# Performance work log

Measured on AMD Instinct MI355X. Metric: run time of the kernel, lower is better.

## Reference

```python
import jax, jax.numpy as jnp
import numpy as np

B, N, T_OBS, N_HEAD = 64, 512, 8, 4
IN_FEAT = T_OBS * 2          # 16
OUT_FEAT = IN_FEAT * 4       # 64 (GAT out / MLP in)
HID1, HID2 = 1024, 512
S, NSAMP = 2, 20
OUT_DIM = S * NSAMP          # 40


def setup_inputs() -> dict:
    key = jax.random.key(0)
    ks = jax.random.split(key, 12)
    x = jax.random.normal(ks[0], (B, N, T_OBS, 2), dtype=jnp.float32)
    # binary adjacency-style mask over the dense node-node attention
    mask = (jax.random.uniform(ks[1], (B, 1, N, N)) > 0.1).astype(jnp.float32)
    xav = lambda k, shp, fi, fo: jax.random.uniform(k, shp, jnp.float32, -1.0, 1.0) * (1.414 * np.sqrt(6.0 / (fi + fo)))
    w = xav(ks[2], (N_HEAD, IN_FEAT, OUT_FEAT), IN_FEAT, OUT_FEAT)
    a_src = xav(ks[3], (N_HEAD, OUT_FEAT, 1), OUT_FEAT, 1)
    a_dst = xav(ks[4], (N_HEAD, OUT_FEAT, 1), OUT_FEAT, 1)
    bias = jnp.zeros((OUT_FEAT,), jnp.float32)
    lin = lambda k, fi, fo: jax.random.uniform(k, (fi, fo), jnp.float32, -1.0, 1.0) * np.sqrt(1.0 / fi)
    W1 = lin(ks[5], OUT_FEAT, HID1); b1 = jnp.zeros((HID1,), jnp.float32)
    W2 = lin(ks[6], HID1, HID2);     b2 = jnp.zeros((HID2,), jnp.float32)
    W3 = lin(ks[7], HID2, OUT_DIM);  b3 = jnp.zeros((OUT_DIM,), jnp.float32)
    return {"x": x, "mask": mask, "w": w, "a_src": a_src, "a_dst": a_dst,
            "bias": bias, "W1": W1, "b1": b1, "W2": W2, "b2": b2, "W3": W3, "b3": b3}


def reference(x, mask, w, a_src, a_dst, bias, W1, b1, W2, b2, W3, b3):
    b, n = x.shape[0], x.shape[1]
    node = x.reshape(b, n, -1)                                   # [B,N,16]
    # per-head projection: [B,N,16] x [H,16,64] -> [B,H,N,64]
    h_prime = jnp.einsum('bni,hio->bhno', node, w)
    attn_src = jnp.einsum('bhno,ho->bhn', h_prime, a_src[..., 0])
    attn_dst = jnp.einsum('bhno,ho->bhn', h_prime, a_dst[..., 0])
    attn = attn_src[..., :, None] * attn_dst[..., None, :]       # [B,H,N,N] outer product
    attn = jnp.where(attn >= 0, attn, 0.2 * attn)                # leaky_relu(0.2)
    attn = jax.nn.softmax(attn, axis=-1)
    # dropout is identity in eval mode
    attn = attn * mask
    out = jnp.einsum('bhnm,bhmo->bno', attn, h_prime) + bias     # sum over heads fused
    out = out + h_prime.sum(axis=1)                              # skip connection
    # MLP: activation BEFORE each linear (as in original MLP.forward)
    y = out
    for W, bb in ((W1, b1), (W2, b2), (W3, b3)):
        y = jax.nn.relu(y) @ W + bb
    y = y.reshape(b, n, NSAMP, -1)[..., 0:S]                     # [B,N,20,2]
    return jnp.clip(jax.nn.sigmoid(y), 0.01, 0.99)
```

## Files before the change

### kernel.cpp

```cpp
#include <hip/hip_runtime.h>
#include <math.h>

typedef short bf16x8 __attribute__((ext_vector_type(8)));
typedef float f32x4 __attribute__((ext_vector_type(4)));

#define BB 64
#define NN 512
#define NH 4
#define FI 16
#define FO 64
#define HD1 1024
#define HD2 512
#define ODIM 40

__device__ __forceinline__ unsigned short f2bf(float f) {
    unsigned u = __float_as_uint(f);
    u += 0x7fffu + ((u >> 16) & 1u);
    return (unsigned short)(u >> 16);
}
__device__ __forceinline__ unsigned pack2(float a, float b) {
    return (unsigned)f2bf(a) | ((unsigned)f2bf(b) << 16);
}
__device__ __forceinline__ void gload16(const void* g, void* l) {
    __builtin_amdgcn_global_load_lds(
        (const __attribute__((address_space(1))) unsigned int*)g,
        (__attribute__((address_space(3))) unsigned int*)l,
        16, 0, 0);
}

__global__ void k_wa(const float* __restrict__ w, const float* __restrict__ a_src,
                     const float* __restrict__ a_dst, float* __restrict__ wa)
{
    int t = threadIdx.x;
    int h = t >> 4;
    float s = 0.f, d = 0.f;
    for (int o = 0; o < FO; ++o) {
        float wv = w[t*FO + o];
        s = fmaf(wv, a_src[h*FO + o], s);
        d = fmaf(wv, a_dst[h*FO + o], d);
    }
    wa[t] = s; wa[64 + t] = d;
}

__global__ __launch_bounds__(256) void k_proj2(
    const float* __restrict__ x, const float* __restrict__ w,
    const float* __restrict__ bias, const float* __restrict__ wa,
    short* __restrict__ hpT,
    float* __restrict__ asrc, float* __restrict__ adst,
    float* __restrict__ gat)
{
    __shared__ float xS[64][20];
    __shared__ float gS[NH][64][64];
    int b = blockIdx.y;
    int n0 = blockIdx.x * 64;
    int t = threadIdx.x;
    int h = t >> 6, o = t & 63;
    {
        int n = t >> 2, q = t & 3;
        float4 v = *(const float4*)&x[((size_t)b*NN + n0 + n)*FI + q*4];
        *(float4*)&xS[n][q*4] = v;
    }
    float wreg[16];
#pragma unroll
    for (int i = 0; i < FI; ++i) wreg[i] = w[(h*FI + i)*FO + o];
    __syncthreads();

    size_t hbase = ((size_t)(b*NH + h)*FO + o) * NN + n0;
    for (int nc = 0; nc < 8; ++nc) {
        float acc[8];
#pragma unroll
        for (int k = 0; k < 8; ++k) {
            int n = nc*8 + k;
            float4 a0 = *(const float4*)&xS[n][0];
            float4 a1 = *(const float4*)&xS[n][4];
            float4 a2 = *(const float4*)&xS[n][8];
            float4 a3 = *(const float4*)&xS[n][12];
            float sA = fmaf(a0.x, wreg[0], fmaf(a0.y, wreg[1], fmaf(a0.z, wreg[2], a0.w*wreg[3])));
            float sB = fmaf(a1.x, wreg[4], fmaf(a1.y, wreg[5], fmaf(a1.z, wreg[6], a1.w*wreg[7])));
            float sC = fmaf(a2.x, wreg[8], fmaf(a2.y, wreg[9], fmaf(a2.z, wreg[10], a2.w*wreg[11])));
            float sD = fmaf(a3.x, wreg[12], fmaf(a3.y, wreg[13], fmaf(a3.z, wreg[14], a3.w*wreg[15])));
            float s = (sA + sB) + (sC + sD);
            acc[k] = s;
            gS[h][n][o] = s;
        }
        uint4 p;
        p.x = pack2(acc[0], acc[1]); p.y = pack2(acc[2], acc[3]);
        p.z = pack2(acc[4], acc[5]); p.w = pack2(acc[6], acc[7]);
        *(uint4*)&hpT[hbase + nc*8] = p;
    }
    {
        int n = o;
        float vs = 0.f, vd = 0.f;
#pragma unroll
        for (int i = 0; i < FI; ++i) {
            float xv = xS[n][i];
            vs = fmaf(xv, wa[h*FI + i], vs);
            vd = fmaf(xv, wa[64 + h*FI + i], vd);
        }
        asrc[(size_t)(b*NH + h)*NN + n0 + n] = vs;
        adst[(size_t)(b*NH + h)*NN + n0 + n] = vd;
    }
    __syncthreads();
#pragma unroll
    for (int r = 0; r < 16; ++r) {
        int idx = t + r*256;
        int n = idx >> 6, oo = idx & 63;
        float g = bias[oo] + ((gS[0][n][oo] + gS[1][n][oo]) + (gS[2][n][oo] + gS[3][n][oo]));
        gat[((size_t)b*NN + n0 + n)*FO + oo] = g;
    }
}

__global__ __launch_bounds__(256) void k_attn2(
    const short* __restrict__ hpT, const float* __restrict__ mask,
    const float* __restrict__ asrc, const float* __restrict__ adst,
    float* __restrict__ gat)
{
    __shared__ float dS[NH*NN];
    __shared__ char vts[16384];
    __shared__ float dmaxS[NH], dminS[NH];
    int b = blockIdx.y;
    int i0blk = blockIdx.x * 64;
    int t = threadIdx.x;
#pragma unroll
    for (int r = 0; r < 8; ++r) {
        int idx = t + r*256;
        dS[idx] = adst[(size_t)b*(NH*NN) + idx];
    }
    __syncthreads();
    int wv = t >> 6, lane = t & 63;
    {
        float mx = -INFINITY, mn = INFINITY;
        const float* dh = &dS[wv*NN];
#pragma unroll
        for (int q = 0; q < 8; ++q) {
            float v = dh[lane*8 + q];
            mx = fmaxf(mx, v); mn = fminf(mn, v);
        }
#pragma unroll
        for (int off = 1; off < 64; off <<= 1) {
            mx = fmaxf(mx, __shfl_xor(mx, off));
            mn = fminf(mn, __shfl_xor(mn, off));
        }
        if (lane == 0) { dmaxS[wv] = mx; dminS[wv] = mn; }
    }
    __syncthreads();
    int li = lane & 15, kq = lane >> 4;
    int i = i0blk + wv*16 + li;
    float s[NH], m[NH], Ssum[NH];
#pragma unroll
    for (int h = 0; h < NH; ++h) {
        s[h] = asrc[(size_t)(b*NH + h)*NN + i];
        float dm = s[h] >= 0.f ? dmaxS[h] : dminS[h];
        float l = s[h] * dm;
        m[h] = fmaxf(l, 0.2f*l);
        Ssum[h] = 0.f;
    }
    f32x4 accH[NH][4];
#pragma unroll
    for (int h = 0; h < NH; ++h)
#pragma unroll
        for (int ot = 0; ot < 4; ++ot) accH[h][ot] = (f32x4)0.f;

    const float* mrow = &mask[((size_t)b*NN + i)*NN];
    for (int jt = 0; jt < 16; ++jt) {
        int j0 = jt*32;
#pragma unroll
        for (int q = 0; q < 4; ++q) {
            int flatB = wv*4096 + q*1024 + lane*16;
            int row = flatB >> 6;
            int slotS = ((flatB >> 4) & 3) ^ ((row >> 1) & 3);
            const short* src = hpT + ((size_t)b*256 + row)*NN + j0 + slotS*8;
            gload16(src, vts + wv*4096 + q*1024);
        }
        __syncthreads();
        float4 mk0 = *(const float4*)&mrow[j0 + kq*8];
        float4 mk1 = *(const float4*)&mrow[j0 + kq*8 + 4];
        float mk[8] = {mk0.x, mk0.y, mk0.z, mk0.w, mk1.x, mk1.y, mk1.z, mk1.w};
#pragma unroll
        for (int h = 0; h < NH; ++h) {
            float4 d0 = *(const float4*)&dS[h*NN + j0 + kq*8];
            float4 d1 = *(const float4*)&dS[h*NN + j0 + kq*8 + 4];
            float dv[8] = {d0.x,d0.y,d0.z,d0.w,d1.x,d1.y,d1.z,d1.w};
            float u[8];
#pragma unroll
            for (int q = 0; q < 8; ++q) {
                float v = s[h]*dv[q];
                v = fmaxf(v, 0.2f*v);
                u[q] = __expf(v - m[h]);
            }
            Ssum[h] += ((u[0]+u[1]) + (u[2]+u[3])) + ((u[4]+u[5]) + (u[6]+u[7]));
            union { bf16x8 v; unsigned uu[4]; } pf;
#pragma unroll
            for (int q = 0; q < 4; ++q)
                pf.uu[q] = pack2(u[2*q]*mk[2*q], u[2*q+1]*mk[2*q+1]);
#pragma unroll
            for (int ot = 0; ot < 4; ++ot) {
                int row = h*64 + ot*16 + li;
                int slot = kq ^ ((row >> 1) & 3);
                bf16x8 vf = *(bf16x8*)(vts + row*64 + slot*16);
                accH[h][ot] = __builtin_amdgcn_mfma_f32_16x16x32_bf16(pf.v, vf, accH[h][ot], 0, 0, 0);
            }
        }
        __syncthreads();
    }
#pragma unroll
    for (int h = 0; h < NH; ++h) {
        Ssum[h] += __shfl_xor(Ssum[h], 16);
        Ssum[h] += __shfl_xor(Ssum[h], 32);
    }
    float rinv[NH][4];
#pragma unroll
    for (int h = 0; h < NH; ++h)
#pragma unroll
        for (int g = 0; g < 4; ++g)
            rinv[h][g] = 1.0f / __shfl(Ssum[h], kq*4 + g);
#pragma unroll
    for (int ot = 0; ot < 4; ++ot) {
#pragma unroll
        for (int g = 0; g < 4; ++g) {
            int ii = i0blk + wv*16 + kq*4 + g;
            int oo = ot*16 + li;
            size_t ix = ((size_t)b*NN + ii)*FO + oo;
            float add = accH[0][ot][g]*rinv[0][g] + accH[1][ot][g]*rinv[1][g]
                      + accH[2][ot][g]*rinv[2][g] + accH[3][ot][g]*rinv[3][g];
            gat[ix] += add;
        }
    }
}

__global__ __launch_bounds__(256) void k_conv(
    const float* __restrict__ W1, const float* __restrict__ W2, const float* __restrict__ W3,
    short* __restrict__ w1t, short* __restrict__ w2t, short* __restrict__ w3t)
{
    int idx = blockIdx.x * 256 + threadIdx.x;
    if (idx < HD1*FO) {
        int n = idx >> 6, k = idx & 63;
        w1t[idx] = (short)f2bf(W1[k*HD1 + n]);
    } else if (idx < HD1*FO + HD2*HD1) {
        int i2 = idx - HD1*FO;
        int n = i2 >> 10, k = i2 & 1023;
        w2t[i2] = (short)f2bf(W2[k*HD2 + n]);
    } else if (idx < HD1*FO + HD2*HD1 + 48*HD2) {
        int i3 = idx - (HD1*FO + HD2*HD1);
        int n = i3 >> 9, k = i3 & 511;
        w3t[i3] = (short)(n < ODIM ? f2bf(W3[k*ODIM + n]) : 0);
    }
}

__global__ __launch_bounds__(256, 2) void k_mlpA(
    const float* __restrict__ gat,
    const short* __restrict__ w1t, const float* __restrict__ b1,
    short* __restrict__ h1g)
{
    __shared__ char a0b[8192];
    int t = threadIdx.x;
    int lane = t & 63, wave = t >> 6;
    int li = lane & 15, kq = lane >> 4;
    int m0 = blockIdx.x * 64;

    {
        int row = t >> 2, c0 = (t & 3) * 16;
        const float4* g = (const float4*)&gat[(size_t)(m0 + row) * FO + c0];
        float4 v0 = g[0], v1 = g[1], v2 = g[2], v3 = g[3];
        uint4 p0, p1;
        p0.x = pack2(fmaxf(v0.x,0.f), fmaxf(v0.y,0.f));
        p0.y = pack2(fmaxf(v0.z,0.f), fmaxf(v0.w,0.f));
        p0.z = pack2(fmaxf(v1.x,0.f), fmaxf(v1.y,0.f));
        p0.w = pack2(fmaxf(v1.z,0.f), fmaxf(v1.w,0.f));
        p1.x = pack2(fmaxf(v2.x,0.f), fmaxf(v2.y,0.f));
        p1.y = pack2(fmaxf(v2.z,0.f), fmaxf(v2.w,0.f));
        p1.z = pack2(fmaxf(v3.x,0.f), fmaxf(v3.y,0.f));
        p1.w = pack2(fmaxf(v3.z,0.f), fmaxf(v3.w,0.f));
        int base = row*128 + c0*2;
        *(uint4*)(a0b + (base ^ ((row&7)<<4)))      = p0;
        *(uint4*)(a0b + ((base+16) ^ ((row&7)<<4))) = p1;
    }
    __syncthreads();

    for (int c = 0; c < 4; ++c) {
        int n0 = wave * 256 + c * 64;
        f32x4 acc[4][4];
#pragma unroll
        for (int mt = 0; mt < 4; ++mt)
#pragma unroll
            for (int nt = 0; nt < 4; ++nt) acc[mt][nt] = (f32x4)0.f;
#pragma unroll
        for (int ks = 0; ks < 2; ++ks) {
            int k0 = ks * 32;
            bf16x8 xf[4];
#pragma unroll
            for (int mt = 0; mt < 4; ++mt) {
                int row = mt * 16 + li;
                int addr = (row * 128 + k0 * 2 + kq * 16) ^ ((row & 7) << 4);
                xf[mt] = *(bf16x8*)(a0b + addr);
            }
#pragma unroll
            for (int nt = 0; nt < 4; ++nt) {
                int col = n0 + nt * 16 + li;
                bf16x8 wf = *(const bf16x8*)(w1t + col * 64 + k0 + kq * 8);
#pragma unroll
                for (int mt = 0; mt < 4; ++mt)
                    acc[mt][nt] = __builtin_amdgcn_mfma_f32_16x16x32_bf16(wf, xf[mt], acc[mt][nt], 0, 0, 0);
            }
        }
#pragma unroll
        for (int mt = 0; mt < 4; ++mt)
#pragma unroll
            for (int nt = 0; nt < 4; ++nt) {
                int m = mt * 16 + li;
                int nb = n0 + nt * 16 + kq * 4;
                float4 bb = *(const float4*)&b1[nb];
                float v0 = fmaxf(acc[mt][nt][0] + bb.x, 0.f);
                float v1 = fmaxf(acc[mt][nt][1] + bb.y, 0.f);
                float v2 = fmaxf(acc[mt][nt][2] + bb.z, 0.f);
                float v3 = fmaxf(acc[mt][nt][3] + bb.w, 0.f);
                uint2 pw; pw.x = pack2(v0, v1); pw.y = pack2(v2, v3);
                *(uint2*)&h1g[(size_t)(m0 + m) * HD1 + nb] = pw;
            }
    }
}

#define BUFSZ 40960
__global__ __launch_bounds__(512, 2) void k_mlpB(
    const short* __restrict__ h1g,
    const short* __restrict__ w2t, const float* __restrict__ b2,
    const short* __restrict__ w3t, const float* __restrict__ b3,
    float* __restrict__ out)
{
    extern __shared__ char smem[];
    int t = threadIdx.x;
    int lane = t & 63, wave = t >> 6;
    int li = lane & 15, kq = lane >> 4;
    int m0 = blockIdx.x * 128;

    auto STAGE = [&](int i, int ks) {
        char* base = smem + i * BUFSZ;
        {
            int row = wave * 16 + (lane >> 2);
            int slotS = (lane & 3) ^ ((row >> 1) & 3);
            const short* src = h1g + (size_t)(m0 + row) * HD1 + ks * 32 + slotS * 8;
            gload16(src, base + wave * 1024);
        }
#pragma unroll
        for (int q = 0; q < 4; ++q) {
            int flatB = wave * 4096 + q * 1024 + lane * 16;
            int n = flatB >> 6;
            int slotS = ((flatB >> 4) & 3) ^ ((n >> 1) & 3);
            const short* src = w2t + (size_t)n * HD1 + ks * 32 + slotS * 8;
            gload16(src, base + 8192 + wave * 4096 + q * 1024);
        }
    };

    f32x4 acc2[8][4];
#pragma unroll
    for (int mt = 0; mt < 8; ++mt)
#pragma unroll
        for (int nt = 0; nt < 4; ++nt) acc2[mt][nt] = (f32x4)0.f;

    STAGE(0, 0);
    STAGE(1, 1);
    for (int ks = 0; ks < 32; ++ks) {
        int cur = ks & 1;
        if (ks < 31) { asm volatile("s_waitcnt vmcnt(5)" ::: "memory"); }
        else         { asm volatile("s_waitcnt vmcnt(0)" ::: "memory"); }
        __builtin_amdgcn_sched_barrier(0);
        __builtin_amdgcn_s_barrier();
        __builtin_amdgcn_sched_barrier(0);

        char* base = smem + cur * BUFSZ;
        bf16x8 xf[8], wf[4];
#pragma unroll
        for (int mt = 0; mt < 8; ++mt) {
            int m = mt * 16 + li;
            int slot = kq ^ ((m >> 1) & 3);
            xf[mt] = *(bf16x8*)(base + m * 64 + slot * 16);
        }
#pragma unroll
        for (int nt = 0; nt < 4; ++nt) {
            int n = wave * 64 + nt * 16 + li;
            int slot = kq ^ ((n >> 1) & 3);
            wf[nt] = *(bf16x8*)(base + 8192 + n * 64 + slot * 16);
        }
        asm volatile("s_waitcnt lgkmcnt(0)" ::: "memory");
        __builtin_amdgcn_sched_barrier(0);
        __builtin_amdgcn_s_barrier();
        __builtin_amdgcn_sched_barrier(0);
        if (ks < 30) STAGE(cur, ks + 2);

#pragma unroll
        for (int nt = 0; nt < 4; ++nt)
#pragma unroll
            for (int mt = 0; mt < 8; ++mt)
                acc2[mt][nt] = __builtin_amdgcn_mfma_f32_16x16x32_bf16(wf[nt], xf[mt], acc2[mt][nt], 0, 0, 0);
    }
    __syncthreads();

#pragma unroll
    for (int mt = 0; mt < 8; ++mt)
#pragma unroll
        for (int nt = 0; nt < 4; ++nt) {
            int m = mt * 16 + li;
            int nb = wave * 64 + nt * 16 + kq * 4;
            float4 bb = *(const float4*)&b2[nb];
            float v0 = fmaxf(acc2[mt][nt][0] + bb.x, 0.f);
            float v1 = fmaxf(acc2[mt][nt][1] + bb.y, 0.f);
            float v2 = fmaxf(acc2[mt][nt][2] + bb.z, 0.f);
            float v3 = fmaxf(acc2[mt][nt][3] + bb.w, 0.f);
            uint2 pw; pw.x = pack2(v0, v1); pw.y = pack2(v2, v3);
            int addr = (m * 1024 + nb * 2) ^ ((m & 7) << 4);
            *(uint2*)(smem + addr) = pw;
        }
    __syncthreads();

    f32x4 acc3[3];
#pragma unroll
    for (int nt = 0; nt < 3; ++nt) acc3[nt] = (f32x4)0.f;
#pragma unroll
    for (int ks = 0; ks < 16; ++ks) {
        int k0 = ks * 32;
        int m = wave * 16 + li;
        int addr = (m * 1024 + k0 * 2 + kq * 16) ^ ((m & 7) << 4);
        bf16x8 xf = *(bf16x8*)(smem + addr);
#pragma unroll
        for (int nt = 0; nt < 3; ++nt) {
            int col = nt * 16 + li;
            bf16x8 wf = *(const bf16x8*)(w3t + col * 512 + k0 + kq * 8);
            acc3[nt] = __builtin_amdgcn_mfma_f32_16x16x32_bf16(wf, xf, acc3[nt], 0, 0, 0);
        }
    }
#pragma unroll
    for (int nt = 0; nt < 3; ++nt)
#pragma unroll
        for (int g = 0; g < 4; ++g) {
            int n = nt * 16 + kq * 4 + g;
            if (n < ODIM) {
                int m = wave * 16 + li;
                float s = acc3[nt][g] + b3[n];
                s = 1.f / (1.f + __expf(-s));
                s = fminf(fmaxf(s, 0.01f), 0.99f);
                out[(size_t)(m0 + m) * ODIM + n] = s;
            }
        }
}

extern "C" void kernel_launch(void* const* d_in, const int* in_sizes, int n_in,
                              void* d_out, int out_size, void* d_ws, size_t ws_size,
                              hipStream_t stream)
{
    const float* x     = (const float*)d_in[0];
    const float* mask  = (const float*)d_in[1];
    const float* w     = (const float*)d_in[2];
    const float* a_src = (const float*)d_in[3];
    const float* a_dst = (const float*)d_in[4];
    const float* bias  = (const float*)d_in[5];
    const float* W1    = (const float*)d_in[6];
    const float* b1    = (const float*)d_in[7];
    const float* W2    = (const float*)d_in[8];
    const float* b2    = (const float*)d_in[9];
    const float* W3    = (const float*)d_in[10];
    const float* b3    = (const float*)d_in[11];
    float* out = (float*)d_out;

    char* p = (char*)d_ws;
    short* h1g = (short*)p;
    short* hpT = (short*)p;  p += (size_t)BB*NH*FO*NN*2;
    float* asrc = (float*)p; p += (size_t)BB*NH*NN*4;
    float* adst = (float*)p; p += (size_t)BB*NH*NN*4;
    p = (char*)d_ws + (size_t)BB*NN*HD1*2;
    float* gat  = (float*)p; p += (size_t)BB*NN*FO*4;
    short* w1t  = (short*)p; p += (size_t)HD1*FO*2;
    short* w2t  = (short*)p; p += (size_t)HD2*HD1*2;
    short* w3t  = (short*)p; p += (size_t)48*HD2*2;
    float* wa   = (float*)p; p += 128*4;

    k_wa   <<<1, 64, 0, stream>>>(w, a_src, a_dst, wa);
    k_conv <<<(HD1*FO + HD2*HD1 + 48*HD2)/256, 256, 0, stream>>>(W1, W2, W3, w1t, w2t, w3t);
    k_proj2<<<dim3(NN/64, BB), 256, 0, stream>>>(x, w, bias, wa, hpT, asrc, adst, gat);
    k_attn2<<<dim3(NN/64, BB), 256, 0, stream>>>(hpT, mask, asrc, adst, gat);
    k_mlpA <<<BB*NN/64, 256, 0, stream>>>(gat, w1t, b1, h1g);
    k_mlpB <<<BB*NN/128, 512, 131072, stream>>>(h1g, w2t, b2, w3t, b3, out);
}
```

Measured before the change: 167.7 us.

## Pre-layout hpT and W2 in MFMA fragment order, load directly from global

The projection kernel now writes hpT tiled per 32-column block, so the attention kernel can read MFMA B-fragments straight from global memory. This removes the LDS staging and the two block barriers per tile. W2 is likewise converted into a fragment-ordered layout, and k_mlpB loads weight fragments directly into registers two steps ahead, keeping only the activation tile in LDS. The aim is less LDS traffic and fewer barriers. The cost is more global and L2 reads, since each wave reloads the weights itself, plus extra registers. The existing vmcnt(5) wait now has to cover a different mix of outstanding loads.

```diff
diff --git a/kernel.cpp b/kernel.cpp
--- a/kernel.cpp
+++ b/kernel.cpp
@@ -65,7 +65,7 @@
     for (int i = 0; i < FI; ++i) wreg[i] = w[(h*FI + i)*FO + o];
     __syncthreads();
 
-    size_t hbase = ((size_t)(b*NH + h)*FO + o) * NN + n0;
+    short* hb = hpT + (size_t)b * (NH*FO*NN);
     for (int nc = 0; nc < 8; ++nc) {
         float acc[8];
 #pragma unroll
@@ -86,7 +86,8 @@
         uint4 p;
         p.x = pack2(acc[0], acc[1]); p.y = pack2(acc[2], acc[3]);
         p.z = pack2(acc[4], acc[5]); p.w = pack2(acc[6], acc[7]);
-        *(uint4*)&hpT[hbase + nc*8] = p;
+        int jt = (n0 >> 5) + (nc >> 2);
+        *(uint4*)&hb[(size_t)(jt*256 + h*64 + o)*32 + (nc & 3)*8] = p;
     }
     {
         int n = o;
@@ -116,7 +117,6 @@
     float* __restrict__ gat)
 {
     __shared__ float dS[NH*NN];
-    __shared__ char vts[16384];
     __shared__ float dmaxS[NH], dminS[NH];
     int b = blockIdx.y;
     int i0blk = blockIdx.x * 64;
@@ -162,17 +162,9 @@
         for (int ot = 0; ot < 4; ++ot) accH[h][ot] = (f32x4)0.f;
 
     const float* mrow = &mask[((size_t)b*NN + i)*NN];
+    const short* vb = hpT + (size_t)b * (NH*FO*NN);
     for (int jt = 0; jt < 16; ++jt) {
         int j0 = jt*32;
-#pragma unroll
-        for (int q = 0; q < 4; ++q) {
-            int flatB = wv*4096 + q*1024 + lane*16;
-            int row = flatB >> 6;
-            int slotS = ((flatB >> 4) & 3) ^ ((row >> 1) & 3);
-            const short* src = hpT + ((size_t)b*256 + row)*NN + j0 + slotS*8;
-            gload16(src, vts + wv*4096 + q*1024);
-        }
-        __syncthreads();
         float4 mk0 = *(const float4*)&mrow[j0 + kq*8];
         float4 mk1 = *(const float4*)&mrow[j0 + kq*8 + 4];
         float mk[8] = {mk0.x, mk0.y, mk0.z, mk0.w, mk1.x, mk1.y, mk1.z, mk1.w};
@@ -195,13 +187,10 @@
                 pf.uu[q] = pack2(u[2*q]*mk[2*q], u[2*q+1]*mk[2*q+1]);
 #pragma unroll
             for (int ot = 0; ot < 4; ++ot) {
-                int row = h*64 + ot*16 + li;
-                int slot = kq ^ ((row >> 1) & 3);
-                bf16x8 vf = *(bf16x8*)(vts + row*64 + slot*16);
+                bf16x8 vf = *(const bf16x8*)&vb[(size_t)(jt*256 + h*64 + ot*16 + li)*32 + kq*8];
                 accH[h][ot] = __builtin_amdgcn_mfma_f32_16x16x32_bf16(pf.v, vf, accH[h][ot], 0, 0, 0);
             }
         }
-        __syncthreads();
     }
 #pragma unroll
     for (int h = 0; h < NH; ++h) {
@@ -230,7 +219,7 @@
 
 __global__ __launch_bounds__(256) void k_conv(
     const float* __restrict__ W1, const float* __restrict__ W2, const float* __restrict__ W3,
-    short* __restrict__ w1t, short* __restrict__ w2t, short* __restrict__ w3t)
+    short* __restrict__ w1t, short* __restrict__ w2f, short* __restrict__ w3t)
 {
     int idx = blockIdx.x * 256 + threadIdx.x;
     if (idx < HD1*FO) {
@@ -238,8 +227,9 @@
         w1t[idx] = (short)f2bf(W1[k*HD1 + n]);
     } else if (idx < HD1*FO + HD2*HD1) {
         int i2 = idx - HD1*FO;
-        int n = i2 >> 10, k = i2 & 1023;
-        w2t[i2] = (short)f2bf(W2[k*HD2 + n]);
+        int e = i2 & 7, kqq = (i2 >> 3) & 3, n = (i2 >> 5) & 511, ks = i2 >> 14;
+        int k = ks*32 + kqq*8 + e;
+        w2f[i2] = (short)f2bf(W2[k*HD2 + n]);
     } else if (idx < HD1*FO + HD2*HD1 + 48*HD2) {
         int i3 = idx - (HD1*FO + HD2*HD1);
         int n = i3 >> 9, k = i3 & 511;
@@ -320,10 +310,9 @@
     }
 }
 
-#define BUFSZ 40960
 __global__ __launch_bounds__(512, 2) void k_mlpB(
     const short* __restrict__ h1g,
-    const short* __restrict__ w2t, const float* __restrict__ b2,
+    const short* __restrict__ w2f, const float* __restrict__ b2,
     const short* __restrict__ w3t, const float* __restrict__ b3,
     float* __restrict__ out)
 {
@@ -334,22 +323,13 @@
     int m0 = blockIdx.x * 128;
 
     auto STAGE = [&](int i, int ks) {
-        char* base = smem + i * BUFSZ;
-        {
-            int row = wave * 16 + (lane >> 2);
-            int slotS = (lane & 3) ^ ((row >> 1) & 3);
-            const short* src = h1g + (size_t)(m0 + row) * HD1 + ks * 32 + slotS * 8;
-            gload16(src, base + wave * 1024);
-        }
-#pragma unroll
-        for (int q = 0; q < 4; ++q) {
-            int flatB = wave * 4096 + q * 1024 + lane * 16;
-            int n = flatB >> 6;
-            int slotS = ((flatB >> 4) & 3) ^ ((n >> 1) & 3);
-            const short* src = w2t + (size_t)n * HD1 + ks * 32 + slotS * 8;
-            gload16(src, base + 8192 + wave * 4096 + q * 1024);
-        }
+        char* base = smem + i * 8192;
+        int row = wave * 16 + (lane >> 2);
+        int slotS = (lane & 3) ^ ((row >> 1) & 3);
+        const short* src = h1g + (size_t)(m0 + row) * HD1 + ks * 32 + slotS * 8;
+        gload16(src, base + wave * 1024);
     };
+    const short* wfbase = w2f + ((size_t)(wave*64 + li)*4 + kq)*8;
 
     f32x4 acc2[8][4];
 #pragma unroll
@@ -357,8 +337,17 @@
 #pragma unroll
         for (int nt = 0; nt < 4; ++nt) acc2[mt][nt] = (f32x4)0.f;
 
+    bf16x8 wf0[4], wf1[4];
+    __builtin_amdgcn_sched_barrier(0);
     STAGE(0, 0);
+#pragma unroll
+    for (int nt = 0; nt < 4; ++nt) wf0[nt] = *(const bf16x8*)(wfbase + 0*16384 + nt*512);
+    __builtin_amdgcn_sched_barrier(0);
     STAGE(1, 1);
+#pragma unroll
+    for (int nt = 0; nt < 4; ++nt) wf1[nt] = *(const bf16x8*)(wfbase + 1*16384 + nt*512);
+    __builtin_amdgcn_sched_barrier(0);
+
     for (int ks = 0; ks < 32; ++ks) {
         int cur = ks & 1;
         if (ks < 31) { asm volatile("s_waitcnt vmcnt(5)" ::: "memory"); }
@@ -367,31 +356,40 @@
         __builtin_amdgcn_s_barrier();
         __builtin_amdgcn_sched_barrier(0);
 
-        char* base = smem + cur * BUFSZ;
-        bf16x8 xf[8], wf[4];
+        char* base = smem + cur * 8192;
+        bf16x8 xf[8];
 #pragma unroll
         for (int mt = 0; mt < 8; ++mt) {
             int m = mt * 16 + li;
             int slot = kq ^ ((m >> 1) & 3);
             xf[mt] = *(bf16x8*)(base + m * 64 + slot * 16);
         }
-#pragma unroll
-        for (int nt = 0; nt < 4; ++nt) {
-            int n = wave * 64 + nt * 16 + li;
-            int slot = kq ^ ((n >> 1) & 3);
-            wf[nt] = *(bf16x8*)(base + 8192 + n * 64 + slot * 16);
-        }
         asm volatile("s_waitcnt lgkmcnt(0)" ::: "memory");
         __builtin_amdgcn_sched_barrier(0);
         __builtin_amdgcn_s_barrier();
         __builtin_amdgcn_sched_barrier(0);
-        if (ks < 30) STAGE(cur, ks + 2);
+
+        bf16x8 wfn[4];
+        if (ks < 30) {
+            STAGE(cur, ks + 2);
+#pragma unroll
+            for (int nt = 0; nt < 4; ++nt)
+                wfn[nt] = *(const bf16x8*)(wfbase + (size_t)(ks+2)*16384 + nt*512);
+        }
+        __builtin_amdgcn_sched_barrier(0);
 
 #pragma unroll
         for (int nt = 0; nt < 4; ++nt)
 #pragma unroll
             for (int mt = 0; mt < 8; ++mt)
-                acc2[mt][nt] = __builtin_amdgcn_mfma_f32_16x16x32_bf16(wf[nt], xf[mt], acc2[mt][nt], 0, 0, 0);
+                acc2[mt][nt] = __builtin_amdgcn_mfma_f32_16x16x32_bf16(wf0[nt], xf[mt], acc2[mt][nt], 0, 0, 0);
+        if (ks < 30) {
+#pragma unroll
+            for (int nt = 0; nt < 4; ++nt) { wf0[nt] = wf1[nt]; wf1[nt] = wfn[nt]; }
+        } else {
+#pragma unroll
+            for (int nt = 0; nt < 4; ++nt) wf0[nt] = wf1[nt];
+        }
     }
     __syncthreads();
 
@@ -469,14 +467,14 @@
     p = (char*)d_ws + (size_t)BB*NN*HD1*2;
     float* gat  = (float*)p; p += (size_t)BB*NN*FO*4;
     short* w1t  = (short*)p; p += (size_t)HD1*FO*2;
-    short* w2t  = (short*)p; p += (size_t)HD2*HD1*2;
+    short* w2f  = (short*)p; p += (size_t)HD2*HD1*2;
     short* w3t  = (short*)p; p += (size_t)48*HD2*2;
     float* wa   = (float*)p; p += 128*4;
 
     k_wa   <<<1, 64, 0, stream>>>(w, a_src, a_dst, wa);
-    k_conv <<<(HD1*FO + HD2*HD1 + 48*HD2)/256, 256, 0, stream>>>(W1, W2, W3, w1t, w2t, w3t);
+    k_conv <<<(HD1*FO + HD2*HD1 + 48*HD2)/256, 256, 0, stream>>>(W1, W2, W3, w1t, w2f, w3t);
     k_proj2<<<dim3(NN/64, BB), 256, 0, stream>>>(x, w, bias, wa, hpT, asrc, adst, gat);
     k_attn2<<<dim3(NN/64, BB), 256, 0, stream>>>(hpT, mask, asrc, adst, gat);
     k_mlpA <<<BB*NN/64, 256, 0, stream>>>(gat, w1t, b1, h1g);
-    k_mlpB <<<BB*NN/128, 512, 131072, stream>>>(h1g, w2t, b2, w3t, b3, out);
-}
+    k_mlpB <<<BB*NN/128, 512, 131072, stream>>>(h1g, w2f, b2, w3t, b3, out);
+}
```

New measurement: 168.3 us. No clear change (+0.4%).
